# Kernel optimization log

Measured on AMD Instinct MI355X. Metric: run time of the kernel, lower is better.

The kernel has to match this reference:

```python
import jax, jax.numpy as jnp
import numpy as np

B, C, N = 32, 1024, 512
OUTDIM = 256
EPS_SQRT = 1e-12   # clamp before sqrt so diagonal zeros stay differentiable
EPS_NORM = 1e-12   # torch F.normalize eps


def setup_inputs() -> dict:
    key = jax.random.key(0)
    k1, k2, k3, k4, k5 = jax.random.split(key, 5)
    xi = jax.random.normal(k1, (B, 256, N), dtype=jnp.float32)
    xh = jax.random.normal(k2, (B, 256, N), dtype=jnp.float32)
    xo = jax.random.normal(k3, (B, C, N), dtype=jnp.float32)
    # LazyLinear(outdim) materializes as Linear(N*N, outdim)
    fan_in = N * N
    bound = 1.0 / np.sqrt(fan_in)
    W = jax.random.uniform(k4, (fan_in, OUTDIM), dtype=jnp.float32, minval=-bound, maxval=bound)
    b = jax.random.uniform(k5, (OUTDIM,), dtype=jnp.float32, minval=-bound, maxval=bound)
    return {"xi": xi, "xh": xh, "xo": xo, "W": W, "b": b}


def reference(xi, xh, xo, W, b):
    # xi, xh are unused by SoGA.forward
    x = jnp.transpose(xo, (0, 2, 1))                 # [B, N, C]
    # similarity (Gram) matrix over points
    S = jnp.einsum('bnc,bmc->bnm', x, x)             # [B, N, N], symmetric
    # pairwise Euclidean distance between rows of S
    sq = jnp.sum(S * S, axis=-1)                     # [B, N]
    G = jnp.einsum('bnk,bmk->bnm', S, S)             # [B, N, N]
    d2 = sq[:, :, None] + sq[:, None, :] - 2.0 * G
    D = jnp.sqrt(jnp.maximum(d2, EPS_SQRT))          # [B, N, N]
    flat = D.reshape(D.shape[0], -1)                 # [B, N*N]
    d_out = flat @ W + b                             # [B, outdim]
    norm = jnp.maximum(jnp.linalg.norm(d_out, axis=-1, keepdims=True), EPS_NORM)
    return d_out / norm
```

## Files before the change

kernel.cpp:

```cpp
#include <hip/hip_runtime.h>

typedef unsigned short ushort_t;
typedef __attribute__((ext_vector_type(8))) unsigned short ushort8;
typedef __attribute__((ext_vector_type(4))) unsigned short ushort4v;
typedef __attribute__((ext_vector_type(8))) __bf16 bf16x8;
typedef __attribute__((ext_vector_type(4))) float f32x4;
typedef __attribute__((ext_vector_type(4))) float f4;
typedef __attribute__((ext_vector_type(4))) unsigned int uint4v;

#define B_ 32
#define C_ 1024
#define N_ 512
#define O_ 256

__device__ inline float bf2f(unsigned short u) {
  unsigned int i = ((unsigned int)u) << 16;
  return __builtin_bit_cast(float, i);
}
__device__ inline unsigned short f2bf(float f) {
  unsigned int i = __builtin_bit_cast(unsigned int, f);
  i += 0x7FFFu + ((i >> 16) & 1u);
  return (unsigned short)(i >> 16);
}

#define DOT2(acc_, a_, b_)                                                  \
  asm("v_dot2_f32_bf16 %0, %1, %2, %0" : "+v"(acc_) : "v"(a_), "v"(b_))
#define CVTPK(dst_, lo_, hi_)                                               \
  asm("v_cvt_pk_bf16_f32 %0, %1, %2" : "=v"(dst_) : "v"(lo_), "v"(hi_))

__device__ inline void gl_lds16(const ushort_t* g, ushort_t* l) {
  __builtin_amdgcn_global_load_lds(
      (const __attribute__((address_space(1))) void*)g,
      (__attribute__((address_space(3))) void*)l, 16, 0, 0);
}

__global__ __launch_bounds__(256) void k_transpose(const float* __restrict__ xo,
                                                   ushort_t* __restrict__ xoT) {
  __shared__ float tile[64][65];
  const int tn = blockIdx.x, tc = blockIdx.y, b = blockIdx.z;
  const int c0 = tc * 64, n0 = tn * 64;
  const int t = threadIdx.x;
  const int tr = t >> 4, tq = t & 15;
  const float* src = xo + ((size_t)b * C_ + c0) * N_ + n0;
#pragma unroll
  for (int p = 0; p < 4; ++p) {
    int c = p * 16 + tr;
    f4 v = *(const f4*)(src + (size_t)c * N_ + tq * 4);
    tile[c][tq * 4 + 0] = v[0];
    tile[c][tq * 4 + 1] = v[1];
    tile[c][tq * 4 + 2] = v[2];
    tile[c][tq * 4 + 3] = v[3];
  }
  __syncthreads();
  ushort_t* dst = xoT + ((size_t)b * N_ + n0) * C_ + c0;
#pragma unroll
  for (int p = 0; p < 4; ++p) {
    int n = p * 16 + tr;
    ushort4v u;
#pragma unroll
    for (int j = 0; j < 4; ++j) u[j] = f2bf(tile[tq * 4 + j][n]);
    *(ushort4v*)(dst + (size_t)n * C_ + tq * 4) = u;
  }
}

template <int KSTEPS, int LDK>
__device__ inline void gemm_main(const ushort_t* __restrict__ Arows,
                                 const ushort_t* __restrict__ Brows,
                                 ushort_t* lds, f32x4 (&acc)[4][4], int t) {
  ushort_t* lds_a = lds;
  ushort_t* lds_b = lds + 8192;
  const int lane = t & 63, w = t >> 6;
  const int wr = w >> 1, wc = w & 1;
  const int l16 = lane & 15, lg = lane >> 4;
  const int srow = w * 32 + (lane >> 2);
  const int skp = (((lane & 3) ^ ((lane >> 3) & 3)) * 8);
  const int lgsw = ((lg ^ ((l16 >> 1) & 3))) * 8;
#define STAGE(s_, buf_)                                                     \
  {                                                                         \
    _Pragma("unroll") for (int j = 0; j < 2; ++j) {                         \
      const int row = srow + j * 16;                                        \
      gl_lds16(Arows + (size_t)row * LDK + (s_)*32 + skp,                   \
               lds_a + (buf_)*4096 + (w * 2 + j) * 512);                    \
      gl_lds16(Brows + (size_t)row * LDK + (s_)*32 + skp,                   \
               lds_b + (buf_)*4096 + (w * 2 + j) * 512);                    \
    }                                                                       \
  }
  STAGE(0, 0)
  __syncthreads();
  int buf = 0;
  for (int s = 0; s < KSTEPS; ++s) {
    if (s + 1 < KSTEPS) STAGE(s + 1, buf ^ 1)
    ushort8 au[4], bu[4];
#pragma unroll
    for (int i = 0; i < 4; ++i) {
      au[i] = *(const ushort8*)&lds_a[buf * 4096 + (wr * 64 + i * 16 + l16) * 32 + lgsw];
      bu[i] = *(const ushort8*)&lds_b[buf * 4096 + (wc * 64 + i * 16 + l16) * 32 + lgsw];
    }
#pragma unroll
    for (int ai = 0; ai < 4; ++ai)
#pragma unroll
      for (int bi = 0; bi < 4; ++bi)
        acc[ai][bi] = __builtin_amdgcn_mfma_f32_16x16x32_bf16(
            __builtin_bit_cast(bf16x8, au[ai]), __builtin_bit_cast(bf16x8, bu[bi]),
            acc[ai][bi], 0, 0, 0);
    __syncthreads();
    buf ^= 1;
  }
#undef STAGE
}

#define CT_LD 136

__global__ __launch_bounds__(256, 3) void k_sgemm(const ushort_t* __restrict__ xoT,
                                                  ushort_t* __restrict__ S) {
  __shared__ ushort_t lds[128 * CT_LD];
  const int b = blockIdx.y, tile = blockIdx.x;
  const int n0 = (tile >> 2) * 128, m0 = (tile & 3) * 128;
  const ushort_t* Ab = xoT + (size_t)b * N_ * C_ + (size_t)n0 * C_;
  const ushort_t* Bb = xoT + (size_t)b * N_ * C_ + (size_t)m0 * C_;
  f32x4 acc[4][4] = {};
  const int t = threadIdx.x;
  gemm_main<C_ / 32, C_>(Ab, Bb, lds, acc, t);
  const int lane = t & 63, w = t >> 6, wr = w >> 1, wc = w & 1;
  const int l16 = lane & 15, lg = lane >> 4;
#pragma unroll
  for (int ai = 0; ai < 4; ++ai)
#pragma unroll
    for (int bi = 0; bi < 4; ++bi)
#pragma unroll
      for (int j = 0; j < 4; ++j) {
        int r = wr * 64 + ai * 16 + lg * 4 + j;
        int c = wc * 64 + bi * 16 + l16;
        lds[r * CT_LD + c] = f2bf(acc[ai][bi][j]);
      }
  __syncthreads();
  ushort_t* Sb = S + (size_t)b * N_ * N_;
#pragma unroll
  for (int p = 0; p < 8; ++p) {
    int id = p * 256 + t;
    int r = id >> 4, cc = (id & 15) * 8;
    *(ushort8*)(Sb + (size_t)(n0 + r) * N_ + m0 + cc) = *(const ushort8*)&lds[r * CT_LD + cc];
  }
}

__global__ __launch_bounds__(256) void k_sq(const ushort_t* __restrict__ S,
                                            float* __restrict__ sq) {
  const int row = blockIdx.x * 4 + (threadIdx.x >> 6);
  const int lane = threadIdx.x & 63;
  ushort8 v = *(const ushort8*)(S + (size_t)row * N_ + lane * 8);
  float q = 0.f;
#pragma unroll
  for (int j = 0; j < 8; ++j) {
    float f = bf2f(v[j]);
    q += f * f;
  }
#pragma unroll
  for (int off = 32; off; off >>= 1) q += __shfl_down(q, off, 64);
  if (lane == 0) sq[row] = q;
}

__global__ __launch_bounds__(256, 3) void k_dgemm(const ushort_t* __restrict__ S,
                                                  const float* __restrict__ sq,
                                                  ushort_t* __restrict__ D) {
  __shared__ ushort_t lds[128 * CT_LD];
  __shared__ float sqn[128], sqm[128];
  const int b = blockIdx.y, tile = blockIdx.x;
  const int n0 = (tile >> 2) * 128, m0 = (tile & 3) * 128;
  const int t = threadIdx.x;
  if (t < 128)
    sqn[t] = sq[b * N_ + n0 + t];
  else
    sqm[t - 128] = sq[b * N_ + m0 + (t - 128)];
  const ushort_t* Ab = S + (size_t)b * N_ * N_ + (size_t)n0 * N_;
  const ushort_t* Bb = S + (size_t)b * N_ * N_ + (size_t)m0 * N_;
  f32x4 acc[4][4] = {};
  gemm_main<N_ / 32, N_>(Ab, Bb, lds, acc, t);
  const int lane = t & 63, w = t >> 6, wr = w >> 1, wc = w & 1;
  const int l16 = lane & 15, lg = lane >> 4;
#pragma unroll
  for (int ai = 0; ai < 4; ++ai)
#pragma unroll
    for (int bi = 0; bi < 4; ++bi)
#pragma unroll
      for (int j = 0; j < 4; ++j) {
        int nl = wr * 64 + ai * 16 + lg * 4 + j;
        int ml = wc * 64 + bi * 16 + l16;
        float d2 = sqn[nl] + sqm[ml] - 2.f * acc[ai][bi][j];
        lds[nl * CT_LD + ml] = f2bf(sqrtf(fmaxf(d2, 1e-12f)));
      }
  __syncthreads();
  ushort_t* Db = D + (size_t)b * N_ * N_;
#pragma unroll
  for (int p = 0; p < 8; ++p) {
    int id = p * 256 + t;
    int r = id >> 4, cc = (id & 15) * 8;
    *(ushort8*)(Db + (size_t)(n0 + r) * N_ + m0 + cc) = *(const ushort8*)&lds[r * CT_LD + cc];
  }
}

__global__ __launch_bounds__(256, 2) void k_dw(const ushort_t* __restrict__ Dm,
                                               const float* __restrict__ W,
                                               float* __restrict__ partial) {
  __shared__ ushort_t lds_d[32 * 512];
  const int g = blockIdx.x, t = threadIdx.x;
  const int k0 = g * 512;
  const int w = t >> 6, lane = t & 63;
#pragma unroll
  for (int i = 0; i < 8; ++i) {
    int c = i * 256 + t;
    gl_lds16(Dm + (size_t)(c >> 6) * (N_ * N_) + k0 + (c & 63) * 8,
             lds_d + (i * 256 + w * 64) * 8);
  }
  __syncthreads();
  const int ks = w;
  const int ob = lane * 4;
  float acc[32][4] = {};
  const float* Wb = W + ((size_t)(k0 + ks * 128)) * O_ + ob;
  const ushort_t* dbase = &lds_d[ks * 128];
  unsigned int wA[4][4], wB[4][4];
#define LOADW(dst, kb_)                                                      \
  {                                                                          \
    _Pragma("unroll") for (int r = 0; r < 4; ++r) {                          \
      f4 e = *(const f4*)(Wb + (size_t)((kb_)*8 + 2 * r) * O_);              \
      f4 o2 = *(const f4*)(Wb + (size_t)((kb_)*8 + 2 * r + 1) * O_);         \
      CVTPK(dst[r][0], e[0], o2[0]);                                         \
      CVTPK(dst[r][1], e[1], o2[1]);                                         \
      CVTPK(dst[r][2], e[2], o2[2]);                                         \
      CVTPK(dst[r][3], e[3], o2[3]);                                         \
    }                                                                        \
  }
#define COMP(kb_, w_)                                                        \
  {                                                                          \
    const int kl = (kb_)*8;                                                  \
    _Pragma("unroll") for (int bb = 0; bb < 32; ++bb) {                      \
      uint4v dv4 = *(const uint4v*)&dbase[bb * 512 + kl];                    \
      _Pragma("unroll") for (int j = 0; j < 4; ++j) {                        \
        DOT2(acc[bb][0], dv4[j], w_[j][0]);                                  \
        DOT2(acc[bb][1], dv4[j], w_[j][1]);                                  \
        DOT2(acc[bb][2], dv4[j], w_[j][2]);                                  \
        DOT2(acc[bb][3], dv4[j], w_[j][3]);                                  \
      }                                                                      \
    }                                                                        \
  }
  LOADW(wA, 0)
#pragma unroll 1
  for (int kb = 0; kb < 16; kb += 2) {
    LOADW(wB, kb + 1)
    COMP(kb, wA)
    if (kb + 2 < 16) LOADW(wA, kb + 2)
    COMP(kb + 1, wB)
  }
#undef LOADW
#undef COMP
  __syncthreads();
  float* lds_f = (float*)lds_d;
#pragma unroll
  for (int c = 0; c < 4; ++c) {
#pragma unroll
    for (int q = 0; q < 8; ++q) {
      f4 v;
      v[0] = acc[c * 8 + q][0];
      v[1] = acc[c * 8 + q][1];
      v[2] = acc[c * 8 + q][2];
      v[3] = acc[c * 8 + q][3];
      *(f4*)&lds_f[(ks * 8 + q) * 256 + lane * 4] = v;
    }
    __syncthreads();
    {
      const int q2 = t >> 5, o = (t & 31) * 8;
      f4 s0 = {}, s1 = {};
#pragma unroll
      for (int k2 = 0; k2 < 4; ++k2) {
        f4 a0 = *(const f4*)&lds_f[(k2 * 8 + q2) * 256 + o];
        f4 a1 = *(const f4*)&lds_f[(k2 * 8 + q2) * 256 + o + 4];
        s0 += a0;
        s1 += a1;
      }
      float* P = partial + ((size_t)g * B_ + c * 8 + q2) * O_ + o;
      *(f4*)P = s0;
      *(f4*)(P + 4) = s1;
    }
    __syncthreads();
  }
}

__global__ __launch_bounds__(256) void k_red1(const float* __restrict__ partial,
                                              float* __restrict__ p2) {
  const int pg = blockIdx.x, b = blockIdx.y, t = threadIdx.x;
  float s = 0.f;
#pragma unroll 8
  for (int p = pg * 64; p < pg * 64 + 64; ++p)
    s += partial[((size_t)p * B_ + b) * O_ + t];
  p2[((size_t)pg * B_ + b) * O_ + t] = s;
}

__global__ __launch_bounds__(256) void k_red2(const float* __restrict__ p2,
                                              const float* __restrict__ bias,
                                              float* __restrict__ out) {
  const int b = blockIdx.x, t = threadIdx.x;
  float s = 0.f;
#pragma unroll
  for (int pg = 0; pg < 8; ++pg) s += p2[((size_t)pg * B_ + b) * O_ + t];
  s += bias[t];
  float q = s * s;
#pragma unroll
  for (int off = 32; off; off >>= 1) q += __shfl_down(q, off, 64);
  __shared__ float lds[4];
  if ((t & 63) == 0) lds[t >> 6] = q;
  __syncthreads();
  float tot = lds[0] + lds[1] + lds[2] + lds[3];
  out[b * O_ + t] = s / fmaxf(sqrtf(tot), 1e-12f);
}

extern "C" void kernel_launch(void* const* d_in, const int* in_sizes, int n_in,
                              void* d_out, int out_size, void* d_ws, size_t ws_size,
                              hipStream_t stream) {
  const float* xo = (const float*)d_in[2];
  const float* W = (const float*)d_in[3];
  const float* bias = (const float*)d_in[4];
  float* out = (float*)d_out;

  char* ws = (char*)d_ws;
  const size_t OFF_S = 33554432, OFF_D = 50331648, OFF_SQ = 67108864,
               OFF_P2 = 67174400, NEED = 67436544;
  if (ws_size < NEED) return;
  ushort_t* xoT = (ushort_t*)ws;
  ushort_t* S = (ushort_t*)(ws + OFF_S);
  ushort_t* D = (ushort_t*)(ws + OFF_D);
  float* sq = (float*)(ws + OFF_SQ);
  float* p2 = (float*)(ws + OFF_P2);
  float* partial = (float*)ws;

  hipLaunchKernelGGL(k_transpose, dim3(8, 16, 32), dim3(256), 0, stream, xo, xoT);
  hipLaunchKernelGGL(k_sgemm, dim3(16, 32), dim3(256), 0, stream, xoT, S);
  hipLaunchKernelGGL(k_sq, dim3(4096), dim3(256), 0, stream, S, sq);
  hipLaunchKernelGGL(k_dgemm, dim3(16, 32), dim3(256), 0, stream, S, sq, D);
  hipLaunchKernelGGL(k_dw, dim3(512), dim3(256), 0, stream, D, W, partial);
  hipLaunchKernelGGL(k_red1, dim3(8, 32), dim3(256), 0, stream, partial, p2);
  hipLaunchKernelGGL(k_red2, dim3(32), dim3(256), 0, stream, p2, bias, out);
}
```

Measured before the change: 148.7 us.

## Split k_dw work over output halves to shrink accumulators and raise occupancy

The D·W kernel now handles 256 K-rows per block instead of 512, launches twice as many blocks, and splits the four waves into two K-halves by two output-column halves. Each thread keeps 32x2 accumulators instead of 32x4, which cuts register pressure and lets launch bounds ask for 4 blocks per CU, with half the LDS per block. The cost is that each D element is read and converted against fewer W columns per LDS load, giving more LDS traffic per FLOP. The partial buffer doubles, so the first reduction pass sums 128 partials per group instead of 64.

Result: slower. 152.0 us (+2.2%).

```diff
diff --git a/kernel.cpp b/kernel.cpp
--- a/kernel.cpp
+++ b/kernel.cpp
@@ -6,6 +6,7 @@
 typedef __attribute__((ext_vector_type(8))) __bf16 bf16x8;
 typedef __attribute__((ext_vector_type(4))) float f32x4;
 typedef __attribute__((ext_vector_type(4))) float f4;
+typedef __attribute__((ext_vector_type(2))) float f2;
 typedef __attribute__((ext_vector_type(4))) unsigned int uint4v;
 
 #define B_ 32
@@ -198,47 +199,44 @@
   }
 }
 
-__global__ __launch_bounds__(256, 2) void k_dw(const ushort_t* __restrict__ Dm,
+__global__ __launch_bounds__(256, 4) void k_dw(const ushort_t* __restrict__ Dm,
                                                const float* __restrict__ W,
                                                float* __restrict__ partial) {
-  __shared__ ushort_t lds_d[32 * 512];
+  __shared__ ushort_t lds_d[32 * 256];
   const int g = blockIdx.x, t = threadIdx.x;
-  const int k0 = g * 512;
+  const int k0 = g * 256;
   const int w = t >> 6, lane = t & 63;
 #pragma unroll
-  for (int i = 0; i < 8; ++i) {
+  for (int i = 0; i < 4; ++i) {
     int c = i * 256 + t;
-    gl_lds16(Dm + (size_t)(c >> 6) * (N_ * N_) + k0 + (c & 63) * 8,
+    gl_lds16(Dm + (size_t)(c >> 5) * (N_ * N_) + k0 + (c & 31) * 8,
              lds_d + (i * 256 + w * 64) * 8);
   }
   __syncthreads();
-  const int ks = w;
-  const int ob = lane * 4;
-  float acc[32][4] = {};
+  const int ks = w & 1;
+  const int oh = w >> 1;
+  const int ob = oh * 128 + lane * 2;
+  float acc[32][2] = {};
   const float* Wb = W + ((size_t)(k0 + ks * 128)) * O_ + ob;
   const ushort_t* dbase = &lds_d[ks * 128];
-  unsigned int wA[4][4], wB[4][4];
+  unsigned int wA[4][2], wB[4][2];
 #define LOADW(dst, kb_)                                                      \
   {                                                                          \
     _Pragma("unroll") for (int r = 0; r < 4; ++r) {                          \
-      f4 e = *(const f4*)(Wb + (size_t)((kb_)*8 + 2 * r) * O_);              \
-      f4 o2 = *(const f4*)(Wb + (size_t)((kb_)*8 + 2 * r + 1) * O_);         \
+      f2 e = *(const f2*)(Wb + (size_t)((kb_)*8 + 2 * r) * O_);              \
+      f2 o2 = *(const f2*)(Wb + (size_t)((kb_)*8 + 2 * r + 1) * O_);         \
       CVTPK(dst[r][0], e[0], o2[0]);                                         \
       CVTPK(dst[r][1], e[1], o2[1]);                                         \
-      CVTPK(dst[r][2], e[2], o2[2]);                                         \
-      CVTPK(dst[r][3], e[3], o2[3]);                                         \
     }                                                                        \
   }
 #define COMP(kb_, w_)                                                        \
   {                                                                          \
     const int kl = (kb_)*8;                                                  \
     _Pragma("unroll") for (int bb = 0; bb < 32; ++bb) {                      \
-      uint4v dv4 = *(const uint4v*)&dbase[bb * 512 + kl];                    \
+      uint4v dv4 = *(const uint4v*)&dbase[bb * 256 + kl];                    \
       _Pragma("unroll") for (int j = 0; j < 4; ++j) {                        \
         DOT2(acc[bb][0], dv4[j], w_[j][0]);                                  \
         DOT2(acc[bb][1], dv4[j], w_[j][1]);                                  \
-        DOT2(acc[bb][2], dv4[j], w_[j][2]);                                  \
-        DOT2(acc[bb][3], dv4[j], w_[j][3]);                                  \
       }                                                                      \
     }                                                                        \
   }
@@ -255,28 +253,23 @@
   __syncthreads();
   float* lds_f = (float*)lds_d;
 #pragma unroll
-  for (int c = 0; c < 4; ++c) {
+  for (int c4 = 0; c4 < 4; ++c4) {
 #pragma unroll
     for (int q = 0; q < 8; ++q) {
-      f4 v;
-      v[0] = acc[c * 8 + q][0];
-      v[1] = acc[c * 8 + q][1];
-      v[2] = acc[c * 8 + q][2];
-      v[3] = acc[c * 8 + q][3];
-      *(f4*)&lds_f[(ks * 8 + q) * 256 + lane * 4] = v;
+      f2 v;
+      v[0] = acc[c4 * 8 + q][0];
+      v[1] = acc[c4 * 8 + q][1];
+      *(f2*)&lds_f[(w * 8 + q) * 128 + lane * 2] = v;
     }
     __syncthreads();
     {
-      const int q2 = t >> 5, o = (t & 31) * 8;
-      f4 s0 = {}, s1 = {};
-#pragma unroll
-      for (int k2 = 0; k2 < 4; ++k2) {
-        f4 a0 = *(const f4*)&lds_f[(k2 * 8 + q2) * 256 + o];
-        f4 a1 = *(const f4*)&lds_f[(k2 * 8 + q2) * 256 + o + 4];
-        s0 += a0;
-        s1 += a1;
-      }
-      float* P = partial + ((size_t)g * B_ + c * 8 + q2) * O_ + o;
+      const int q2 = t >> 5, o8 = (t & 31) * 8;
+      const int ohh = o8 >> 7, ol = o8 & 127;
+      f4 s0 = *(const f4*)&lds_f[((ohh * 2 + 0) * 8 + q2) * 128 + ol];
+      f4 s1 = *(const f4*)&lds_f[((ohh * 2 + 0) * 8 + q2) * 128 + ol + 4];
+      s0 += *(const f4*)&lds_f[((ohh * 2 + 1) * 8 + q2) * 128 + ol];
+      s1 += *(const f4*)&lds_f[((ohh * 2 + 1) * 8 + q2) * 128 + ol + 4];
+      float* P = partial + ((size_t)g * B_ + c4 * 8 + q2) * O_ + o8;
       *(f4*)P = s0;
       *(f4*)(P + 4) = s1;
     }
@@ -289,7 +282,7 @@
   const int pg = blockIdx.x, b = blockIdx.y, t = threadIdx.x;
   float s = 0.f;
 #pragma unroll 8
-  for (int p = pg * 64; p < pg * 64 + 64; ++p)
+  for (int p = pg * 128; p < pg * 128 + 128; ++p)
     s += partial[((size_t)p * B_ + b) * O_ + t];
   p2[((size_t)pg * B_ + b) * O_ + t] = s;
 }
@@ -335,7 +328,7 @@
   hipLaunchKernelGGL(k_sgemm, dim3(16, 32), dim3(256), 0, stream, xoT, S);
   hipLaunchKernelGGL(k_sq, dim3(4096), dim3(256), 0, stream, S, sq);
   hipLaunchKernelGGL(k_dgemm, dim3(16, 32), dim3(256), 0, stream, S, sq, D);
-  hipLaunchKernelGGL(k_dw, dim3(512), dim3(256), 0, stream, D, W, partial);
+  hipLaunchKernelGGL(k_dw, dim3(1024), dim3(256), 0, stream, D, W, partial);
   hipLaunchKernelGGL(k_red1, dim3(8, 32), dim3(256), 0, stream, partial, p2);
   hipLaunchKernelGGL(k_red2, dim3(32), dim3(256), 0, stream, p2, bias, out);
 }
```
